# Optimization experiments

Measured on AMD Instinct MI355X. Metric: run time of the kernel, lower is better.

The kernel has to match this reference:

```python
import jax, jax.numpy as jnp
import numpy as np

PATCH_WEIGHT = 0.5  # module init kwarg
B, C, H = 2, 4, 128  # vol dims (H=W=D)
N, P = 128, 32       # num patches total, patch edge (Hp=Wp=Dp)


def setup_inputs() -> dict:
    key = jax.random.key(0)
    k1, k2, k3 = jax.random.split(key, 3)
    patches = jax.random.normal(k1, (N, C, P, P, P), dtype=jnp.float32)
    vol = jax.random.normal(k2, (B, C, H, H, H), dtype=jnp.float32)
    # lower bound in [0, H-P] so the PxPxP slice stays in-bounds; center = lower + P//2
    crop_centers = jax.random.randint(k3, (N, 3), 0, H - P + 1, dtype=jnp.int32) + P // 2
    return {"patches": patches, "vol": vol, "crop_centers": crop_centers}


def reference(patches, vol, crop_centers):
    n, c_dim, p = patches.shape[0], patches.shape[1], patches.shape[2]
    b_dim = vol.shape[0]
    num_patch_per_batch = n // b_dim
    b_idx = jnp.arange(n) // num_patch_per_batch            # [N] batch index per patch
    lo = crop_centers - p // 2                              # [N,3] slice lower bounds
    offs = jnp.arange(p)
    hi = lo[:, 0, None] + offs                              # [N,P]
    wi = lo[:, 1, None] + offs                              # [N,P]
    di = lo[:, 2, None] + offs                              # [N,P]
    c_idx = jnp.arange(c_dim)
    # module: new_vol = vol*(1-pw); w_t is overwritten with ones, so add pw*patch
    new_vol = vol * (1.0 - PATCH_WEIGHT)
    new_vol = new_vol.at[
        b_idx[:, None, None, None, None],
        c_idx[None, :, None, None, None],
        hi[:, None, :, None, None],
        wi[:, None, None, :, None],
        di[:, None, None, None, :],
    ].add(patches * PATCH_WEIGHT)                           # scatter-add handles overlaps
    return new_vol
```

## Files before the change

kernel.cpp:

```cpp
#include <hip/hip_runtime.h>


constexpr int C = 4, H = 128, P = 32;
constexpr int NPB  = 64;
constexpr int PCH4 = P * P * P / 4;

__global__ __launch_bounds__(256) void patch_gather_kernel(
        const float4* __restrict__ patches4,
        const int*   __restrict__ centers,
        const float4* __restrict__ vol4,
        float4* __restrict__ out4) {
    int blk = blockIdx.x;
    int wgrp = blk & 15;
    int h    = (blk >> 4) & 127;
    int c    = (blk >> 11) & 3;
    int b    = blk >> 13;
    int tid  = threadIdx.x;

    int w0 = wgrp << 3;
    int d4 = tid & 31;
    int w  = w0 + (tid >> 5);
    int d0 = d4 << 2;

    int base4 = (((b * C + c) * H + h) * H + w) * 32 + d4;
    float4 v = vol4[base4];

    int lane = tid & 63;
    int cb   = (b * NPB + lane) * 3;
    int lo0  = centers[cb + 0] - 16;
    int lo1  = centers[cb + 1] - 16;
    int lo2  = centers[cb + 2] - 16;
    bool cand = ((unsigned)(h - lo0) < 32u) &&
                ((unsigned)(w0 - lo1 + 7) < 39u);
    int packed = ((h - lo0) << 14) | (lo1 << 7) | lo2;
    unsigned long long mask = __ballot(cand);

    float4 acc = make_float4(0.f, 0.f, 0.f, 0.f);
    const float4* pbat = patches4 + ((size_t)b * NPB * C + c) * PCH4;

    while (mask) {
        int l = __ffsll((long long)mask) - 1;
        mask &= mask - 1;
        int e = __shfl(packed, l);
        int hi   = (e >> 14) & 31;
        int plo1 = (e >> 7) & 127;
        int plo2 = e & 127;
        int wi = w - plo1;
        int k0 = d0 - plo2;
        bool hit = ((unsigned)wi < 32u) && (k0 > -4) && (k0 < 32);

        float4 z = make_float4(0.f, 0.f, 0.f, 0.f);
        float4 A = z, Bv = z;
        if (hit) {
            int q = (k0 + 4) >> 2;
            int ka = q - 1, kb = q;
            const float4* pr = pbat + (size_t)l * C * PCH4 + (hi * 32 + wi) * 8;
            if ((unsigned)ka < 8u) A  = pr[ka];
            if ((unsigned)kb < 8u) Bv = pr[kb];
        }
        int shift = __builtin_amdgcn_readfirstlane(k0 & 3);
        switch (shift) {
        case 0:
            acc.x += A.x; acc.y += A.y; acc.z += A.z; acc.w += A.w; break;
        case 1:
            acc.x += A.y; acc.y += A.z; acc.z += A.w; acc.w += Bv.x; break;
        case 2:
            acc.x += A.z; acc.y += A.w; acc.z += Bv.x; acc.w += Bv.y; break;
        default:
            acc.x += A.w; acc.y += Bv.x; acc.z += Bv.y; acc.w += Bv.z; break;
        }
    }

    float4 o;
    o.x = (v.x + acc.x) * 0.5f;
    o.y = (v.y + acc.y) * 0.5f;
    o.z = (v.z + acc.z) * 0.5f;
    o.w = (v.w + acc.w) * 0.5f;
    out4[base4] = o;
}

extern "C" void kernel_launch(void* const* d_in, const int* in_sizes, int n_in,
                              void* d_out, int out_size, void* d_ws, size_t ws_size,
                              hipStream_t stream) {
    const float* patches = (const float*)d_in[0];
    const float* vol     = (const float*)d_in[1];
    const int*   centers = (const int*)d_in[2];
    float* out = (float*)d_out;

    patch_gather_kernel<<<16384, 256, 0, stream>>>(
        (const float4*)patches, centers, (const float4*)vol, (float4*)out);
}
```

Before: 57.19 us.

## Split candidate patches across four wavefronts and reduce via shared memory

Each block now covers only two w-rows (64 float4 outputs) instead of eight. Its four wavefronts divide the candidate-patch loop round-robin, and the partial sums are combined through LDS before one wave writes the output. The aim is more parallelism per output and a shorter serial candidate loop per wave, which helps latency hiding. In exchange the grid is four times larger, each wave recomputes the center loads and ballot, and the kernel adds a __syncthreads and an LDS reduction.

```diff
diff --git a/kernel.cpp b/kernel.cpp
--- a/kernel.cpp
+++ b/kernel.cpp
@@ -10,73 +10,89 @@
         const int*   __restrict__ centers,
         const float4* __restrict__ vol4,
         float4* __restrict__ out4) {
+    __shared__ float4 sacc[3][64];
+
     int blk = blockIdx.x;
-    int wgrp = blk & 15;
-    int h    = (blk >> 4) & 127;
-    int c    = (blk >> 11) & 3;
-    int b    = blk >> 13;
+    int wp   = blk & 63;
+    int h    = (blk >> 6) & 127;
+    int c    = (blk >> 13) & 3;
+    int b    = blk >> 15;
     int tid  = threadIdx.x;
+    int lane = tid & 63;
+    int widx = tid >> 6;
 
-    int w0 = wgrp << 3;
-    int d4 = tid & 31;
-    int w  = w0 + (tid >> 5);
-    int d0 = d4 << 2;
+    int wlo = wp << 1;
+    int d4  = lane & 31;
+    int w   = wlo + (lane >> 5);
+    int d0  = d4 << 2;
 
     int base4 = (((b * C + c) * H + h) * H + w) * 32 + d4;
-    float4 v = vol4[base4];
+    float4 v = make_float4(0.f, 0.f, 0.f, 0.f);
+    if (widx == 0) v = vol4[base4];
 
-    int lane = tid & 63;
-    int cb   = (b * NPB + lane) * 3;
-    int lo0  = centers[cb + 0] - 16;
-    int lo1  = centers[cb + 1] - 16;
-    int lo2  = centers[cb + 2] - 16;
+    int cb  = (b * NPB + lane) * 3;
+    int lo0 = centers[cb + 0] - 16;
+    int lo1 = centers[cb + 1] - 16;
+    int lo2 = centers[cb + 2] - 16;
     bool cand = ((unsigned)(h - lo0) < 32u) &&
-                ((unsigned)(w0 - lo1 + 7) < 39u);
+                ((unsigned)(wlo - lo1 + 1) < 33u);
     int packed = ((h - lo0) << 14) | (lo1 << 7) | lo2;
     unsigned long long mask = __ballot(cand);
 
     float4 acc = make_float4(0.f, 0.f, 0.f, 0.f);
     const float4* pbat = patches4 + ((size_t)b * NPB * C + c) * PCH4;
 
+    int j = 0;
     while (mask) {
         int l = __ffsll((long long)mask) - 1;
         mask &= mask - 1;
-        int e = __shfl(packed, l);
-        int hi   = (e >> 14) & 31;
-        int plo1 = (e >> 7) & 127;
-        int plo2 = e & 127;
-        int wi = w - plo1;
-        int k0 = d0 - plo2;
-        bool hit = ((unsigned)wi < 32u) && (k0 > -4) && (k0 < 32);
+        if ((j & 3) == widx) {
+            int e = __shfl(packed, l);
+            int hi   = (e >> 14) & 31;
+            int plo1 = (e >> 7) & 127;
+            int plo2 = e & 127;
+            int wi = w - plo1;
+            int k0 = d0 - plo2;
+            bool hit = ((unsigned)wi < 32u) && (k0 > -4) && (k0 < 32);
 
-        float4 z = make_float4(0.f, 0.f, 0.f, 0.f);
-        float4 A = z, Bv = z;
-        if (hit) {
-            int q = (k0 + 4) >> 2;
-            int ka = q - 1, kb = q;
-            const float4* pr = pbat + (size_t)l * C * PCH4 + (hi * 32 + wi) * 8;
-            if ((unsigned)ka < 8u) A  = pr[ka];
-            if ((unsigned)kb < 8u) Bv = pr[kb];
+            float4 z = make_float4(0.f, 0.f, 0.f, 0.f);
+            float4 A = z, Bv = z;
+            if (hit) {
+                int q = (k0 + 4) >> 2;
+                int ka = q - 1, kb = q;
+                const float4* pr = pbat + (size_t)l * C * PCH4
+                                 + (hi * 32 + wi) * 8;
+                if ((unsigned)ka < 8u) A  = pr[ka];
+                if ((unsigned)kb < 8u) Bv = pr[kb];
+            }
+            int shift = __builtin_amdgcn_readfirstlane(k0 & 3);
+            switch (shift) {
+            case 0:
+                acc.x += A.x; acc.y += A.y; acc.z += A.z; acc.w += A.w; break;
+            case 1:
+                acc.x += A.y; acc.y += A.z; acc.z += A.w; acc.w += Bv.x; break;
+            case 2:
+                acc.x += A.z; acc.y += A.w; acc.z += Bv.x; acc.w += Bv.y; break;
+            default:
+                acc.x += A.w; acc.y += Bv.x; acc.z += Bv.y; acc.w += Bv.z; break;
+            }
         }
-        int shift = __builtin_amdgcn_readfirstlane(k0 & 3);
-        switch (shift) {
-        case 0:
-            acc.x += A.x; acc.y += A.y; acc.z += A.z; acc.w += A.w; break;
-        case 1:
-            acc.x += A.y; acc.y += A.z; acc.z += A.w; acc.w += Bv.x; break;
-        case 2:
-            acc.x += A.z; acc.y += A.w; acc.z += Bv.x; acc.w += Bv.y; break;
-        default:
-            acc.x += A.w; acc.y += Bv.x; acc.z += Bv.y; acc.w += Bv.z; break;
-        }
+        ++j;
     }
 
-    float4 o;
-    o.x = (v.x + acc.x) * 0.5f;
-    o.y = (v.y + acc.y) * 0.5f;
-    o.z = (v.z + acc.z) * 0.5f;
-    o.w = (v.w + acc.w) * 0.5f;
-    out4[base4] = o;
+    if (widx > 0) sacc[widx - 1][lane] = acc;
+    __syncthreads();
+    if (widx == 0) {
+        float4 p0 = sacc[0][lane];
+        float4 p1 = sacc[1][lane];
+        float4 p2 = sacc[2][lane];
+        float4 o;
+        o.x = (v.x + acc.x + p0.x + p1.x + p2.x) * 0.5f;
+        o.y = (v.y + acc.y + p0.y + p1.y + p2.y) * 0.5f;
+        o.z = (v.z + acc.z + p0.z + p1.z + p2.z) * 0.5f;
+        o.w = (v.w + acc.w + p0.w + p1.w + p2.w) * 0.5f;
+        out4[base4] = o;
+    }
 }
 
 extern "C" void kernel_launch(void* const* d_in, const int* in_sizes, int n_in,
@@ -87,6 +103,6 @@
     const int*   centers = (const int*)d_in[2];
     float* out = (float*)d_out;
 
-    patch_gather_kernel<<<16384, 256, 0, stream>>>(
+    patch_gather_kernel<<<65536, 256, 0, stream>>>(
         (const float4*)patches, centers, (const float4*)vol, (float4*)out);
 }
```

New measurement: 82.64 us. 1.44x slower.

## Batch four candidate patch loads per iteration and tighten wavefront candidate filter

Applied to the files above, without the earlier changes.

The candidate test now uses the wavefront's actual two-row w range instead of the whole 8-row block, so fewer patches are iterated per wave. The candidate loop is unrolled by four with clamped, unconditional loads, and masks applied through fmaf, so several gathers can be in flight at once. This trades extra loads of unused data and more registers for better memory-level parallelism.

```diff
diff --git a/kernel.cpp b/kernel.cpp
--- a/kernel.cpp
+++ b/kernel.cpp
@@ -30,8 +30,9 @@
     int lo0  = centers[cb + 0] - 16;
     int lo1  = centers[cb + 1] - 16;
     int lo2  = centers[cb + 2] - 16;
+    int wlo  = w0 + ((tid >> 6) << 1);
     bool cand = ((unsigned)(h - lo0) < 32u) &&
-                ((unsigned)(w0 - lo1 + 7) < 39u);
+                ((unsigned)(wlo - lo1 + 1) < 33u);
     int packed = ((h - lo0) << 14) | (lo1 << 7) | lo2;
     unsigned long long mask = __ballot(cand);
 
@@ -39,35 +40,62 @@
     const float4* pbat = patches4 + ((size_t)b * NPB * C + c) * PCH4;
 
     while (mask) {
-        int l = __ffsll((long long)mask) - 1;
-        mask &= mask - 1;
-        int e = __shfl(packed, l);
-        int hi   = (e >> 14) & 31;
-        int plo1 = (e >> 7) & 127;
-        int plo2 = e & 127;
-        int wi = w - plo1;
-        int k0 = d0 - plo2;
-        bool hit = ((unsigned)wi < 32u) && (k0 > -4) && (k0 < 32);
-
-        float4 z = make_float4(0.f, 0.f, 0.f, 0.f);
-        float4 A = z, Bv = z;
-        if (hit) {
-            int q = (k0 + 4) >> 2;
-            int ka = q - 1, kb = q;
-            const float4* pr = pbat + (size_t)l * C * PCH4 + (hi * 32 + wi) * 8;
-            if ((unsigned)ka < 8u) A  = pr[ka];
-            if ((unsigned)kb < 8u) Bv = pr[kb];
+        float4 A[4], Bv[4];
+        int   k0v[4];
+        float hitf[4];
+        int   shv[4];
+        #pragma unroll
+        for (int s = 0; s < 4; ++s) {
+            bool has = (mask != 0ull);
+            int l_  = __ffsll((long long)mask) - 1;
+            mask &= mask - 1ull;
+            int lc  = has ? l_ : 0;
+            int e   = __shfl(packed, lc);
+            int hi   = (e >> 14) & 31;
+            int plo1 = (e >> 7) & 127;
+            int plo2 = e & 127;
+            int wi = w - plo1;
+            int k0 = d0 - plo2;
+            bool hit = has && ((unsigned)wi < 32u) && (k0 > -4) && (k0 < 32);
+            int wic = min(max(wi, 0), 31);
+            int q   = min(max((k0 + 4) >> 2, 0), 8);
+            int ka  = max(q - 1, 0);
+            int kb  = min(q, 7);
+            const float4* pr = pbat + (size_t)lc * C * PCH4
+                             + (hi * 32 + wic) * 8;
+            A[s]  = pr[ka];
+            Bv[s] = pr[kb];
+            k0v[s]  = k0;
+            hitf[s] = hit ? 1.0f : 0.0f;
+            shv[s]  = k0 & 3;
         }
-        int shift = __builtin_amdgcn_readfirstlane(k0 & 3);
-        switch (shift) {
-        case 0:
-            acc.x += A.x; acc.y += A.y; acc.z += A.z; acc.w += A.w; break;
-        case 1:
-            acc.x += A.y; acc.y += A.z; acc.z += A.w; acc.w += Bv.x; break;
-        case 2:
-            acc.x += A.z; acc.y += A.w; acc.z += Bv.x; acc.w += Bv.y; break;
-        default:
-            acc.x += A.w; acc.y += Bv.x; acc.z += Bv.y; acc.w += Bv.z; break;
+        #pragma unroll
+        for (int s = 0; s < 4; ++s) {
+            int shift = __builtin_amdgcn_readfirstlane(shv[s]);
+            int k0 = k0v[s];
+            float m0 = ((unsigned)(k0 + 0) < 32u) ? hitf[s] : 0.0f;
+            float m1 = ((unsigned)(k0 + 1) < 32u) ? hitf[s] : 0.0f;
+            float m2 = ((unsigned)(k0 + 2) < 32u) ? hitf[s] : 0.0f;
+            float m3 = ((unsigned)(k0 + 3) < 32u) ? hitf[s] : 0.0f;
+            float4 Aa = A[s], Bb = Bv[s];
+            switch (shift) {
+            case 0:
+                acc.x = fmaf(m0, Aa.x, acc.x); acc.y = fmaf(m1, Aa.y, acc.y);
+                acc.z = fmaf(m2, Aa.z, acc.z); acc.w = fmaf(m3, Aa.w, acc.w);
+                break;
+            case 1:
+                acc.x = fmaf(m0, Aa.y, acc.x); acc.y = fmaf(m1, Aa.z, acc.y);
+                acc.z = fmaf(m2, Aa.w, acc.z); acc.w = fmaf(m3, Bb.x, acc.w);
+                break;
+            case 2:
+                acc.x = fmaf(m0, Aa.z, acc.x); acc.y = fmaf(m1, Aa.w, acc.y);
+                acc.z = fmaf(m2, Bb.x, acc.z); acc.w = fmaf(m3, Bb.y, acc.w);
+                break;
+            default:
+                acc.x = fmaf(m0, Aa.w, acc.x); acc.y = fmaf(m1, Bb.x, acc.y);
+                acc.z = fmaf(m2, Bb.y, acc.z); acc.w = fmaf(m3, Bb.z, acc.w);
+                break;
+            }
         }
     }
 
```

After: 82.36 us. 1.44x slower.
